# Kernel optimization log

Measured on AMD Instinct MI355X. Metric: run time of the kernel, lower is better.

Reference implementation:

```python
import jax, jax.numpy as jnp
import numpy as np

B, S, D, H = 2, 2048, 1024, 16
DK = D // H


def setup_inputs() -> dict:
    key = jax.random.key(0)
    ks = jax.random.split(key, 8)
    q = jax.random.normal(ks[0], (B, S, D), dtype=jnp.float32)
    k = jax.random.normal(ks[1], (B, S, D), dtype=jnp.float32)
    v = jax.random.normal(ks[2], (B, S, D), dtype=jnp.float32)
    mask = jax.random.randint(ks[3], (B, 1, S, S), 0, 2, dtype=jnp.int32)
    sc = 1.0 / np.sqrt(D)
    Wq = jax.random.normal(ks[4], (D, D), dtype=jnp.float32) * sc
    Wk = jax.random.normal(ks[5], (D, D), dtype=jnp.float32) * sc
    Wv = jax.random.normal(ks[6], (D, D), dtype=jnp.float32) * sc
    Wo = jax.random.normal(ks[7], (D, D), dtype=jnp.float32) * sc
    return {"q": q, "k": k, "v": v, "mask": mask, "Wq": Wq, "Wk": Wk, "Wv": Wv, "Wo": Wo}


def reference(q, k, v, mask, Wq, Wk, Wv, Wo):
    # Linear projections (torch Linear: x @ W.T; bias=False). Weights here stored
    # as [D, D] applied as x @ W (equivalent parameterization).
    query = q @ Wq  # [B,S,D]
    key = k @ Wk
    value = v @ Wv
    # split heads -> [B,H,S,DK]
    query = query.reshape(B, S, H, DK).transpose(0, 2, 1, 3)
    key = key.reshape(B, S, H, DK).transpose(0, 2, 1, 3)
    value = value.reshape(B, S, H, DK).transpose(0, 2, 1, 3)
    scores = jnp.einsum('bhqd,bhkd->bhqk', query, key) / jnp.sqrt(jnp.float32(DK))
    scores = jnp.where(mask == 0, jnp.float32(-1e9), scores)
    probs = jax.nn.softmax(scores, axis=-1)  # dropout p=0.0 -> identity
    x = jnp.einsum('bhqk,bhkd->bhqd', probs, value)
    x = x.transpose(0, 2, 1, 3).reshape(B, S, D)
    return x @ Wo
```

## Files before the change

kernel.cpp:

```cpp
#include <hip/hip_runtime.h>
#include <hip/hip_bf16.h>
#include <math.h>

#define B_ 2
#define S_ 2048
#define D_ 1024
#define H_ 16
#define DK_ 64
#define SW_ (S_ / 64)

typedef unsigned short u16;
typedef unsigned int u32;
typedef unsigned long long u64;
typedef __attribute__((ext_vector_type(8))) short short8;
typedef __attribute__((ext_vector_type(4))) float float4_;
typedef __attribute__((ext_vector_type(4))) unsigned int uint4_;

static __device__ inline u16 f_to_bf16(float f) {
    union { float f; u32 i; } x; x.f = f;
    u32 r = x.i + 0x7fff + ((x.i >> 16) & 1);
    return (u16)(r >> 16);
}

static __device__ __forceinline__ u32 pack2(float a, float b) {
    union { float f; u32 i; } xa, xb; xa.f = a; xb.f = b;
    return ((xa.i + 0x8000u) >> 16) | ((xb.i + 0x8000u) & 0xffff0000u);
}

static __device__ __forceinline__ u32 cvtpk(float a, float b) {
    u32 r;
    asm("v_cvt_pk_bf16_f32 %0, %1, %2" : "=v"(r) : "v"(a), "v"(b));
    return r;
}

static __device__ __forceinline__ float fast_exp2(float x) {
#if __has_builtin(__builtin_amdgcn_exp2f)
    return __builtin_amdgcn_exp2f(x);
#else
    return exp2f(x);
#endif
}

static __device__ inline void gl_lds16(const u16* g, u16* l) {
    __builtin_amdgcn_global_load_lds((const __attribute__((address_space(1))) void*)g,
                                     (__attribute__((address_space(3))) void*)l, 16, 0, 0);
}

__global__ __launch_bounds__(256) void prep(const float* __restrict__ q,
                                            const float* __restrict__ k,
                                            const float* __restrict__ v,
                                            const int* __restrict__ mask,
                                            const float* __restrict__ W0,
                                            const float* __restrict__ W1,
                                            const float* __restrict__ W2,
                                            const float* __restrict__ W3,
                                            u16* __restrict__ qb, u16* __restrict__ kb,
                                            u16* __restrict__ vb,
                                            u16* __restrict__ T0, u16* __restrict__ T1,
                                            u16* __restrict__ T2, u16* __restrict__ T3,
                                            u64* __restrict__ mpk) {
    __shared__ float tile[32][33];
    int gx = blockIdx.x, tid = threadIdx.x;
    if (gx < 6144) {
        int z = gx >> 11;
        int bx = gx & 2047;
        const float* s = (z == 0) ? q : ((z == 1) ? k : v);
        u16* d = (z == 0) ? qb : ((z == 1) ? kb : vb);
        int i = (bx * 256 + tid) * 8;
        #pragma unroll
        for (int j = 0; j < 8; ++j) d[i + j] = f_to_bf16(s[i + j]);
    } else if (gx < 10240) {
        int g2 = gx - 6144;
        int z = g2 >> 10;
        int rem = g2 & 1023;
        const float* W = (z == 0) ? W0 : ((z == 1) ? W1 : ((z == 2) ? W2 : W3));
        u16* Wt = (z == 0) ? T0 : ((z == 1) ? T1 : ((z == 2) ? T2 : T3));
        int k0 = (rem >> 5) * 32, n0 = (rem & 31) * 32;
        int tx = tid & 31, ty = tid >> 5;
        #pragma unroll
        for (int i2 = 0; i2 < 4; ++i2) {
            int row = ty + i2 * 8;
            tile[row][tx] = W[(size_t)(k0 + row) * D_ + n0 + tx];
        }
        __syncthreads();
        #pragma unroll
        for (int i2 = 0; i2 < 4; ++i2) {
            int row = ty + i2 * 8;
            Wt[(size_t)(n0 + row) * D_ + k0 + tx] = f_to_bf16(tile[tx][row]);
        }
    } else {
        int g3 = gx - 10240;
        int wv = (g3 * 256 + tid) >> 6;
        int lane = tid & 63;
        #pragma unroll
        for (int i2 = 0; i2 < 8; ++i2) {
            int wd = wv * 8 + i2;
            u64 bits = __ballot(mask[(size_t)wd * 64 + lane] != 0);
            if (lane == 0) mpk[wd] = bits;
        }
    }
}

static __device__ __forceinline__ void gemm128_body(u16* lds,
                                                    const u16* __restrict__ A,
                                                    const u16* __restrict__ Bt,
                                                    int K, float4_ (&acc)[4][4]) {
    u16* ldsA = lds;
    u16* ldsB = lds + 4096;
    int tm = blockIdx.x, tn = blockIdx.y;
    int t = threadIdx.x, l = t & 63;
    int w = t >> 6, wr = w >> 1, wc = w & 1;
    int colL = l & 15, grp = l >> 4;
    int sw4 = (grp ^ ((colL >> 1) & 3)) << 3;
    int f0 = t, f1 = t + 256;
    int row0 = f0 >> 2, kc0 = (((f0 & 3) ^ ((f0 >> 3) & 3)) << 3);
    int row1 = f1 >> 2, kc1 = (((f1 & 3) ^ ((f1 >> 3) & 3)) << 3);
    const u16* gA0 = A  + (size_t)(tm * 128 + row0) * K + kc0;
    const u16* gA1 = A  + (size_t)(tm * 128 + row1) * K + kc1;
    const u16* gB0 = Bt + (size_t)(tn * 128 + row0) * K + kc0;
    const u16* gB1 = Bt + (size_t)(tn * 128 + row1) * K + kc1;

    #pragma unroll
    for (int mi = 0; mi < 4; ++mi)
        #pragma unroll
        for (int ni = 0; ni < 4; ++ni)
            acc[mi][ni] = (float4_){0.f, 0.f, 0.f, 0.f};

    for (int k0 = 0; k0 < K; k0 += 32) {
        __syncthreads();
        gl_lds16(gA0 + k0, ldsA + f0 * 8);
        gl_lds16(gA1 + k0, ldsA + f1 * 8);
        gl_lds16(gB0 + k0, ldsB + f0 * 8);
        gl_lds16(gB1 + k0, ldsB + f1 * 8);
        __syncthreads();
        short8 a[4], b[4];
        #pragma unroll
        for (int mi = 0; mi < 4; ++mi)
            a[mi] = *(const short8*)&ldsA[(wr * 64 + mi * 16 + colL) * 32 + sw4];
        #pragma unroll
        for (int ni = 0; ni < 4; ++ni)
            b[ni] = *(const short8*)&ldsB[(wc * 64 + ni * 16 + colL) * 32 + sw4];
        #pragma unroll
        for (int mi = 0; mi < 4; ++mi)
            #pragma unroll
            for (int ni = 0; ni < 4; ++ni)
                acc[mi][ni] = __builtin_amdgcn_mfma_f32_16x16x32_bf16(a[mi], b[ni], acc[mi][ni], 0, 0, 0);
    }
}

__global__ __launch_bounds__(256, 3) void gemm_qkv(const u16* __restrict__ qb,
                                                   const u16* __restrict__ kb,
                                                   const u16* __restrict__ vb,
                                                   const u16* __restrict__ Wqt,
                                                   const u16* __restrict__ Wkt,
                                                   const u16* __restrict__ Wvt,
                                                   u16* __restrict__ Qp,
                                                   u16* __restrict__ Kp,
                                                   u16* __restrict__ Vt) {
    __shared__ u16 lds[8192];
    int z = blockIdx.z;
    const u16* A  = (z == 0) ? qb  : ((z == 1) ? kb  : vb);
    const u16* Bt = (z == 0) ? Wqt : ((z == 1) ? Wkt : Wvt);
    float4_ acc[4][4];
    gemm128_body(lds, A, Bt, D_, acc);

    int tm = blockIdx.x, tn = blockIdx.y;
    int t = threadIdx.x, l = t & 63;
    int w = t >> 6, wr = w >> 1, wc = w & 1;
    int colL = l & 15, grp = l >> 4;

    if (z < 2) {
        u16* Y = (z == 0) ? Qp : Kp;
        float sc = (z == 0) ? (0.125f * 1.44269504f) : 1.0f;
        #pragma unroll
        for (int mi = 0; mi < 4; ++mi)
            #pragma unroll
            for (int ni = 0; ni < 4; ++ni)
                #pragma unroll
                for (int r = 0; r < 4; ++r)
                    Y[(size_t)(tm * 128 + wr * 64 + mi * 16 + grp * 4 + r) * D_
                      + tn * 128 + wc * 64 + ni * 16 + colL] = f_to_bf16(acc[mi][ni][r] * sc);
    } else {
        int tok_base = tm * 128 + wr * 64;
        int bb = tok_base >> 11;
        int s_hi = tok_base & (S_ - 1);
        #pragma unroll
        for (int mi = 0; mi < 4; ++mi)
            #pragma unroll
            for (int ni = 0; ni < 4; ++ni) {
                int n  = tn * 128 + wc * 64 + ni * 16 + colL;
                int hh = n >> 6, dk = n & 63;
                u16* vp = Vt + ((size_t)(bb * H_ + hh) * DK_ + dk) * S_ + s_hi;
                #pragma unroll
                for (int r = 0; r < 4; ++r) {
                    int m = mi * 16 + grp * 4 + r;
                    int mp_ = ((m >> 5) & 1) * 32 + ((m >> 2) & 3) * 8 + ((m >> 4) & 1) * 4 + (m & 3);
                    vp[mp_] = f_to_bf16(acc[mi][ni][r]);
                }
            }
    }
}

__global__ __launch_bounds__(256, 3) void gemm_out(const u16* __restrict__ Xa,
                                                   const u16* __restrict__ Wot,
                                                   float* __restrict__ out) {
    __shared__ u16 lds[8192];
    float4_ acc[4][4];
    gemm128_body(lds, Xa, Wot, out ? (int)D_ : (int)D_, acc);

    int tm = blockIdx.x, tn = blockIdx.y;
    int t = threadIdx.x, l = t & 63;
    int w = t >> 6, wr = w >> 1, wc = w & 1;
    int colL = l & 15, grp = l >> 4;
    #pragma unroll
    for (int mi = 0; mi < 4; ++mi)
        #pragma unroll
        for (int ni = 0; ni < 4; ++ni)
            #pragma unroll
            for (int r = 0; r < 4; ++r)
                out[(size_t)(tm * 128 + wr * 64 + mi * 16 + grp * 4 + r) * D_
                    + tn * 128 + wc * 64 + ni * 16 + colL] = acc[mi][ni][r];
}

__global__ __launch_bounds__(256, 4) void attn128(const u16* __restrict__ Qp,
                                                  const u16* __restrict__ Kp,
                                                  const u16* __restrict__ Vt,
                                                  const u64* __restrict__ mp,
                                                  u16* __restrict__ Xa) {
    __shared__ u16 ldsK[128 * 64];
    __shared__ u16 ldsV[2 * 64 * 64];

    int bid = blockIdx.x;
    int qt = bid & 31, h = (bid >> 5) & 15, b = bid >> 9;
    int t = threadIdx.x, l = t & 63, w = t >> 6;
    int colL = l & 15, grp = l >> 4;

    const u16* qbase = Qp + (size_t)(b * S_ + qt * 64 + w * 16 + colL) * D_ + h * DK_;
    short8 qf0 = *(const short8*)(qbase + grp * 8);
    short8 qf1 = *(const short8*)(qbase + 32 + grp * 8);

    const u16* gK[4];
    const u16* gV[4];
    #pragma unroll
    for (int i = 0; i < 4; ++i) {
        int f = t + 256 * i;
        int krow = f >> 3, kch = (((f & 7) ^ (krow & 7)) << 3);
        gK[i] = Kp + (size_t)(b * S_ + krow) * D_ + h * DK_ + kch;
        int hreg = f >> 9, fp = f & 511;
        int vrow = fp >> 3, vch = (((fp & 7) ^ (vrow & 7)) << 3);
        gV[i] = Vt + ((size_t)(b * H_ + h) * DK_ + vrow) * S_ + hreg * 64 + vch;
    }

    int sw8 = (grp ^ (colL & 7)) << 3;

    short8 onesb;
    #pragma unroll
    for (int j = 0; j < 8; ++j) onesb[j] = (short)0x3F80;

    float4_ lacc = (float4_){0.f, 0.f, 0.f, 0.f};
    float4_ o[4];
    #pragma unroll
    for (int nt = 0; nt < 4; ++nt) o[nt] = (float4_){0.f, 0.f, 0.f, 0.f};

    const u64* mrow = mp + (size_t)(b * S_ + qt * 64 + w * 16 + colL) * SW_;

    for (int kt = 0; kt < S_; kt += 128) {
        u64 mw0 = mrow[(kt >> 6)];
        u64 mw1 = mrow[(kt >> 6) + 1];

        __syncthreads();
        #pragma unroll
        for (int i = 0; i < 4; ++i) {
            int f = t + 256 * i;
            gl_lds16(gK[i] + (size_t)kt * D_, ldsK + f * 8);
            gl_lds16(gV[i] + kt,              ldsV + f * 8);
        }
        __syncthreads();

        float4_ s[8];
        __builtin_amdgcn_s_setprio(1);
        #pragma unroll
        for (int nt = 0; nt < 8; ++nt) {
            int ro = (nt * 16 + colL) * 64;
            short8 kf0 = *(const short8*)&ldsK[ro + sw8];
            short8 kf1 = *(const short8*)&ldsK[ro + (sw8 ^ 32)];
            s[nt] = (float4_){0.f, 0.f, 0.f, 0.f};
            s[nt] = __builtin_amdgcn_mfma_f32_16x16x32_bf16(kf0, qf0, s[nt], 0, 0, 0);
            s[nt] = __builtin_amdgcn_mfma_f32_16x16x32_bf16(kf1, qf1, s[nt], 0, 0, 0);
        }
        __builtin_amdgcn_s_setprio(0);

        u64 msh0 = mw0 >> (grp * 4), msh1 = mw1 >> (grp * 4);
        #pragma unroll
        for (int nt = 0; nt < 8; ++nt) {
            u64 msh = (nt < 4) ? msh0 : msh1;
            #pragma unroll
            for (int r = 0; r < 4; ++r) {
                float p = fast_exp2(s[nt][r]);
                u32 keep = 0u - (u32)((msh >> ((nt & 3) * 16 + r)) & 1ull);
                union { float f; u32 i; } pu; pu.f = p;
                pu.i &= keep;
                s[nt][r] = pu.f;
            }
        }

        short8 pf[4];
        #pragma unroll
        for (int j = 0; j < 4; ++j) {
            uint4_ Ax = { cvtpk(s[2 * j][0], s[2 * j][1]), cvtpk(s[2 * j][2], s[2 * j][3]),
                          cvtpk(s[2 * j + 1][0], s[2 * j + 1][1]), cvtpk(s[2 * j + 1][2], s[2 * j + 1][3]) };
            pf[j] = __builtin_bit_cast(short8, Ax);
        }

        __builtin_amdgcn_s_setprio(1);
        #pragma unroll
        for (int nt = 0; nt < 4; ++nt) {
            int ro = (nt * 16 + colL) * 64;
            short8 vf0 = *(const short8*)&ldsV[ro + sw8];
            short8 vf1 = *(const short8*)&ldsV[ro + (sw8 ^ 32)];
            short8 vf2 = *(const short8*)&ldsV[4096 + ro + sw8];
            short8 vf3 = *(const short8*)&ldsV[4096 + ro + (sw8 ^ 32)];
            o[nt] = __builtin_amdgcn_mfma_f32_16x16x32_bf16(pf[0], vf0, o[nt], 0, 0, 0);
            o[nt] = __builtin_amdgcn_mfma_f32_16x16x32_bf16(pf[1], vf1, o[nt], 0, 0, 0);
            o[nt] = __builtin_amdgcn_mfma_f32_16x16x32_bf16(pf[2], vf2, o[nt], 0, 0, 0);
            o[nt] = __builtin_amdgcn_mfma_f32_16x16x32_bf16(pf[3], vf3, o[nt], 0, 0, 0);
        }
        lacc = __builtin_amdgcn_mfma_f32_16x16x32_bf16(pf[0], onesb, lacc, 0, 0, 0);
        lacc = __builtin_amdgcn_mfma_f32_16x16x32_bf16(pf[1], onesb, lacc, 0, 0, 0);
        lacc = __builtin_amdgcn_mfma_f32_16x16x32_bf16(pf[2], onesb, lacc, 0, 0, 0);
        lacc = __builtin_amdgcn_mfma_f32_16x16x32_bf16(pf[3], onesb, lacc, 0, 0, 0);
        __builtin_amdgcn_s_setprio(0);
    }

    float inv[4];
    #pragma unroll
    for (int r = 0; r < 4; ++r) inv[r] = 1.f / lacc[r];

    u16* xo = Xa + (size_t)(b * S_ + qt * 64 + w * 16 + grp * 4) * D_ + h * DK_;
    #pragma unroll
    for (int r = 0; r < 4; ++r)
        #pragma unroll
        for (int nt = 0; nt < 4; ++nt)
            xo[(size_t)r * D_ + nt * 16 + colL] = f_to_bf16(o[nt][r] * inv[r]);
}

extern "C" void kernel_launch(void* const* d_in, const int* in_sizes, int n_in,
                              void* d_out, int out_size, void* d_ws, size_t ws_size,
                              hipStream_t stream) {
    const float* q    = (const float*)d_in[0];
    const float* k    = (const float*)d_in[1];
    const float* v    = (const float*)d_in[2];
    const int*   mask = (const int*)d_in[3];
    const float* Wq   = (const float*)d_in[4];
    const float* Wk   = (const float*)d_in[5];
    const float* Wv   = (const float*)d_in[6];
    const float* Wo   = (const float*)d_in[7];
    float* out = (float*)d_out;

    const int NQ = B_ * S_ * D_;
    const int NW = D_ * D_;

    u16* qb  = (u16*)d_ws;
    u16* kb  = qb  + NQ;
    u16* vb  = kb  + NQ;
    u16* Wqt = vb  + NQ;
    u16* Wkt = Wqt + NW;
    u16* Wvt = Wkt + NW;
    u16* Wot = Wvt + NW;
    u16* Qp  = Wot + NW;
    u16* Kp  = Qp  + NQ;
    u16* Vt  = Kp  + NQ;
    u16* Xa  = Vt  + NQ;
    u64* mpk = (u64*)(Xa + NQ);

    dim3 cblk(256);
    prep<<<14336, cblk, 0, stream>>>(q, k, v, mask, Wq, Wk, Wv, Wo,
                                     qb, kb, vb, Wqt, Wkt, Wvt, Wot, mpk);

    const int M = B_ * S_;
    gemm_qkv<<<dim3(M / 128, D_ / 128, 3), cblk, 0, stream>>>(qb, kb, vb, Wqt, Wkt, Wvt, Qp, Kp, Vt);

    attn128<<<B_ * H_ * (S_ / 64), cblk, 0, stream>>>(Qp, Kp, Vt, mpk, Xa);

    gemm_out<<<dim3(M / 128, D_ / 128), cblk, 0, stream>>>(Xa, Wot, out);
}
```

Before: 253.7 us.

## Process 128 query rows per attention block to reuse K/V tiles

Each wave now computes two 16-row query groups against the same K and V fragments loaded from shared memory. This halves K/V global-to-LDS loads and LDS fragment reads per query row, and halves the grid size. It doubles accumulator register use, and launch bounds drop to 2 blocks per CU, which reduces occupancy and the number of blocks available to fill the GPU.

```diff
diff --git a/kernel.cpp b/kernel.cpp
--- a/kernel.cpp
+++ b/kernel.cpp
@@ -20,11 +20,6 @@
     union { float f; u32 i; } x; x.f = f;
     u32 r = x.i + 0x7fff + ((x.i >> 16) & 1);
     return (u16)(r >> 16);
-}
-
-static __device__ __forceinline__ u32 pack2(float a, float b) {
-    union { float f; u32 i; } xa, xb; xa.f = a; xb.f = b;
-    return ((xa.i + 0x8000u) >> 16) | ((xb.i + 0x8000u) & 0xffff0000u);
 }
 
 static __device__ __forceinline__ u32 cvtpk(float a, float b) {
@@ -206,7 +201,7 @@
                                                    float* __restrict__ out) {
     __shared__ u16 lds[8192];
     float4_ acc[4][4];
-    gemm128_body(lds, Xa, Wot, out ? (int)D_ : (int)D_, acc);
+    gemm128_body(lds, Xa, Wot, D_, acc);
 
     int tm = blockIdx.x, tn = blockIdx.y;
     int t = threadIdx.x, l = t & 63;
@@ -222,7 +217,7 @@
                     + tn * 128 + wc * 64 + ni * 16 + colL] = acc[mi][ni][r];
 }
 
-__global__ __launch_bounds__(256, 4) void attn128(const u16* __restrict__ Qp,
+__global__ __launch_bounds__(256, 2) void attn128(const u16* __restrict__ Qp,
                                                   const u16* __restrict__ Kp,
                                                   const u16* __restrict__ Vt,
                                                   const u64* __restrict__ mp,
@@ -231,13 +226,16 @@
     __shared__ u16 ldsV[2 * 64 * 64];
 
     int bid = blockIdx.x;
-    int qt = bid & 31, h = (bid >> 5) & 15, b = bid >> 9;
+    int qt = bid & 15, h = (bid >> 4) & 15, b = bid >> 8;
     int t = threadIdx.x, l = t & 63, w = t >> 6;
     int colL = l & 15, grp = l >> 4;
 
-    const u16* qbase = Qp + (size_t)(b * S_ + qt * 64 + w * 16 + colL) * D_ + h * DK_;
-    short8 qf0 = *(const short8*)(qbase + grp * 8);
-    short8 qf1 = *(const short8*)(qbase + 32 + grp * 8);
+    const u16* qbA = Qp + (size_t)(b * S_ + qt * 128 + w * 32 + colL) * D_ + h * DK_;
+    const u16* qbB = qbA + (size_t)16 * D_;
+    short8 qfA0 = *(const short8*)(qbA + grp * 8);
+    short8 qfA1 = *(const short8*)(qbA + 32 + grp * 8);
+    short8 qfB0 = *(const short8*)(qbB + grp * 8);
+    short8 qfB1 = *(const short8*)(qbB + 32 + grp * 8);
 
     const u16* gK[4];
     const u16* gV[4];
@@ -257,16 +255,23 @@
     #pragma unroll
     for (int j = 0; j < 8; ++j) onesb[j] = (short)0x3F80;
 
-    float4_ lacc = (float4_){0.f, 0.f, 0.f, 0.f};
-    float4_ o[4];
-    #pragma unroll
-    for (int nt = 0; nt < 4; ++nt) o[nt] = (float4_){0.f, 0.f, 0.f, 0.f};
-
-    const u64* mrow = mp + (size_t)(b * S_ + qt * 64 + w * 16 + colL) * SW_;
+    float4_ laccA = (float4_){0.f, 0.f, 0.f, 0.f};
+    float4_ laccB = (float4_){0.f, 0.f, 0.f, 0.f};
+    float4_ oA[4], oB[4];
+    #pragma unroll
+    for (int nt = 0; nt < 4; ++nt) {
+        oA[nt] = (float4_){0.f, 0.f, 0.f, 0.f};
+        oB[nt] = (float4_){0.f, 0.f, 0.f, 0.f};
+    }
+
+    const u64* mrA = mp + (size_t)(b * S_ + qt * 128 + w * 32 + colL) * SW_;
+    const u64* mrB = mrA + (size_t)16 * SW_;
 
     for (int kt = 0; kt < S_; kt += 128) {
-        u64 mw0 = mrow[(kt >> 6)];
-        u64 mw1 = mrow[(kt >> 6) + 1];
+        u64 mwA0 = mrA[(kt >> 6)];
+        u64 mwA1 = mrA[(kt >> 6) + 1];
+        u64 mwB0 = mrB[(kt >> 6)];
+        u64 mwB1 = mrB[(kt >> 6) + 1];
 
         __syncthreads();
         #pragma unroll
@@ -277,39 +282,49 @@
         }
         __syncthreads();
 
-        float4_ s[8];
+        float4_ sA[8], sB[8];
         __builtin_amdgcn_s_setprio(1);
         #pragma unroll
         for (int nt = 0; nt < 8; ++nt) {
             int ro = (nt * 16 + colL) * 64;
             short8 kf0 = *(const short8*)&ldsK[ro + sw8];
             short8 kf1 = *(const short8*)&ldsK[ro + (sw8 ^ 32)];
-            s[nt] = (float4_){0.f, 0.f, 0.f, 0.f};
-            s[nt] = __builtin_amdgcn_mfma_f32_16x16x32_bf16(kf0, qf0, s[nt], 0, 0, 0);
-            s[nt] = __builtin_amdgcn_mfma_f32_16x16x32_bf16(kf1, qf1, s[nt], 0, 0, 0);
+            sA[nt] = (float4_){0.f, 0.f, 0.f, 0.f};
+            sA[nt] = __builtin_amdgcn_mfma_f32_16x16x32_bf16(kf0, qfA0, sA[nt], 0, 0, 0);
+            sA[nt] = __builtin_amdgcn_mfma_f32_16x16x32_bf16(kf1, qfA1, sA[nt], 0, 0, 0);
+            sB[nt] = (float4_){0.f, 0.f, 0.f, 0.f};
+            sB[nt] = __builtin_amdgcn_mfma_f32_16x16x32_bf16(kf0, qfB0, sB[nt], 0, 0, 0);
+            sB[nt] = __builtin_amdgcn_mfma_f32_16x16x32_bf16(kf1, qfB1, sB[nt], 0, 0, 0);
         }
         __builtin_amdgcn_s_setprio(0);
 
-        u64 msh0 = mw0 >> (grp * 4), msh1 = mw1 >> (grp * 4);
+        u64 mshA0 = mwA0 >> (grp * 4), mshA1 = mwA1 >> (grp * 4);
+        u64 mshB0 = mwB0 >> (grp * 4), mshB1 = mwB1 >> (grp * 4);
         #pragma unroll
         for (int nt = 0; nt < 8; ++nt) {
-            u64 msh = (nt < 4) ? msh0 : msh1;
+            u32 bitsA = ((u32)((nt < 4 ? mshA0 : mshA1) >> ((nt & 3) * 16))) & 15u;
+            u32 bitsB = ((u32)((nt < 4 ? mshB0 : mshB1) >> ((nt & 3) * 16))) & 15u;
             #pragma unroll
             for (int r = 0; r < 4; ++r) {
-                float p = fast_exp2(s[nt][r]);
-                u32 keep = 0u - (u32)((msh >> ((nt & 3) * 16 + r)) & 1ull);
-                union { float f; u32 i; } pu; pu.f = p;
-                pu.i &= keep;
-                s[nt][r] = pu.f;
+                float pA = fast_exp2(sA[nt][r]);
+                float pB = fast_exp2(sB[nt][r]);
+                u32 keepA = 0u - ((bitsA >> r) & 1u);
+                u32 keepB = 0u - ((bitsB >> r) & 1u);
+                union { float f; u32 i; } ua, ub;
+                ua.f = pA; ua.i &= keepA; sA[nt][r] = ua.f;
+                ub.f = pB; ub.i &= keepB; sB[nt][r] = ub.f;
             }
         }
 
-        short8 pf[4];
+        short8 pfA[4], pfB[4];
         #pragma unroll
         for (int j = 0; j < 4; ++j) {
-            uint4_ Ax = { cvtpk(s[2 * j][0], s[2 * j][1]), cvtpk(s[2 * j][2], s[2 * j][3]),
-                          cvtpk(s[2 * j + 1][0], s[2 * j + 1][1]), cvtpk(s[2 * j + 1][2], s[2 * j + 1][3]) };
-            pf[j] = __builtin_bit_cast(short8, Ax);
+            uint4_ Ax = { cvtpk(sA[2 * j][0], sA[2 * j][1]), cvtpk(sA[2 * j][2], sA[2 * j][3]),
+                          cvtpk(sA[2 * j + 1][0], sA[2 * j + 1][1]), cvtpk(sA[2 * j + 1][2], sA[2 * j + 1][3]) };
+            pfA[j] = __builtin_bit_cast(short8, Ax);
+            uint4_ Bx = { cvtpk(sB[2 * j][0], sB[2 * j][1]), cvtpk(sB[2 * j][2], sB[2 * j][3]),
+                          cvtpk(sB[2 * j + 1][0], sB[2 * j + 1][1]), cvtpk(sB[2 * j + 1][2], sB[2 * j + 1][3]) };
+            pfB[j] = __builtin_bit_cast(short8, Bx);
         }
 
         __builtin_amdgcn_s_setprio(1);
@@ -320,28 +335,42 @@
             short8 vf1 = *(const short8*)&ldsV[ro + (sw8 ^ 32)];
             short8 vf2 = *(const short8*)&ldsV[4096 + ro + sw8];
             short8 vf3 = *(const short8*)&ldsV[4096 + ro + (sw8 ^ 32)];
-            o[nt] = __builtin_amdgcn_mfma_f32_16x16x32_bf16(pf[0], vf0, o[nt], 0, 0, 0);
-            o[nt] = __builtin_amdgcn_mfma_f32_16x16x32_bf16(pf[1], vf1, o[nt], 0, 0, 0);
-            o[nt] = __builtin_amdgcn_mfma_f32_16x16x32_bf16(pf[2], vf2, o[nt], 0, 0, 0);
-            o[nt] = __builtin_amdgcn_mfma_f32_16x16x32_bf16(pf[3], vf3, o[nt], 0, 0, 0);
-        }
-        lacc = __builtin_amdgcn_mfma_f32_16x16x32_bf16(pf[0], onesb, lacc, 0, 0, 0);
-        lacc = __builtin_amdgcn_mfma_f32_16x16x32_bf16(pf[1], onesb, lacc, 0, 0, 0);
-        lacc = __builtin_amdgcn_mfma_f32_16x16x32_bf16(pf[2], onesb, lacc, 0, 0, 0);
-        lacc = __builtin_amdgcn_mfma_f32_16x16x32_bf16(pf[3], onesb, lacc, 0, 0, 0);
+            oA[nt] = __builtin_amdgcn_mfma_f32_16x16x32_bf16(pfA[0], vf0, oA[nt], 0, 0, 0);
+            oA[nt] = __builtin_amdgcn_mfma_f32_16x16x32_bf16(pfA[1], vf1, oA[nt], 0, 0, 0);
+            oA[nt] = __builtin_amdgcn_mfma_f32_16x16x32_bf16(pfA[2], vf2, oA[nt], 0, 0, 0);
+            oA[nt] = __builtin_amdgcn_mfma_f32_16x16x32_bf16(pfA[3], vf3, oA[nt], 0, 0, 0);
+            oB[nt] = __builtin_amdgcn_mfma_f32_16x16x32_bf16(pfB[0], vf0, oB[nt], 0, 0, 0);
+            oB[nt] = __builtin_amdgcn_mfma_f32_16x16x32_bf16(pfB[1], vf1, oB[nt], 0, 0, 0);
+            oB[nt] = __builtin_amdgcn_mfma_f32_16x16x32_bf16(pfB[2], vf2, oB[nt], 0, 0, 0);
+            oB[nt] = __builtin_amdgcn_mfma_f32_16x16x32_bf16(pfB[3], vf3, oB[nt], 0, 0, 0);
+        }
+        laccA = __builtin_amdgcn_mfma_f32_16x16x32_bf16(pfA[0], onesb, laccA, 0, 0, 0);
+        laccA = __builtin_amdgcn_mfma_f32_16x16x32_bf16(pfA[1], onesb, laccA, 0, 0, 0);
+        laccA = __builtin_amdgcn_mfma_f32_16x16x32_bf16(pfA[2], onesb, laccA, 0, 0, 0);
+        laccA = __builtin_amdgcn_mfma_f32_16x16x32_bf16(pfA[3], onesb, laccA, 0, 0, 0);
+        laccB = __builtin_amdgcn_mfma_f32_16x16x32_bf16(pfB[0], onesb, laccB, 0, 0, 0);
+        laccB = __builtin_amdgcn_mfma_f32_16x16x32_bf16(pfB[1], onesb, laccB, 0, 0, 0);
+        laccB = __builtin_amdgcn_mfma_f32_16x16x32_bf16(pfB[2], onesb, laccB, 0, 0, 0);
+        laccB = __builtin_amdgcn_mfma_f32_16x16x32_bf16(pfB[3], onesb, laccB, 0, 0, 0);
         __builtin_amdgcn_s_setprio(0);
     }
 
-    float inv[4];
-    #pragma unroll
-    for (int r = 0; r < 4; ++r) inv[r] = 1.f / lacc[r];
-
-    u16* xo = Xa + (size_t)(b * S_ + qt * 64 + w * 16 + grp * 4) * D_ + h * DK_;
+    float invA[4], invB[4];
+    #pragma unroll
+    for (int r = 0; r < 4; ++r) {
+        invA[r] = 1.f / laccA[r];
+        invB[r] = 1.f / laccB[r];
+    }
+
+    u16* xoA = Xa + (size_t)(b * S_ + qt * 128 + w * 32 + grp * 4) * D_ + h * DK_;
+    u16* xoB = xoA + (size_t)16 * D_;
     #pragma unroll
     for (int r = 0; r < 4; ++r)
         #pragma unroll
-        for (int nt = 0; nt < 4; ++nt)
-            xo[(size_t)r * D_ + nt * 16 + colL] = f_to_bf16(o[nt][r] * inv[r]);
+        for (int nt = 0; nt < 4; ++nt) {
+            xoA[(size_t)r * D_ + nt * 16 + colL] = f_to_bf16(oA[nt][r] * invA[r]);
+            xoB[(size_t)r * D_ + nt * 16 + colL] = f_to_bf16(oB[nt][r] * invB[r]);
+        }
 }
 
 extern "C" void kernel_launch(void* const* d_in, const int* in_sizes, int n_in,
@@ -380,7 +409,7 @@
     const int M = B_ * S_;
     gemm_qkv<<<dim3(M / 128, D_ / 128, 3), cblk, 0, stream>>>(qb, kb, vb, Wqt, Wkt, Wvt, Qp, Kp, Vt);
 
-    attn128<<<B_ * H_ * (S_ / 64), cblk, 0, stream>>>(Qp, Kp, Vt, mpk, Xa);
+    attn128<<<B_ * H_ * (S_ / 128), cblk, 0, stream>>>(Qp, Kp, Vt, mpk, Xa);
 
     gemm_out<<<dim3(M / 128, D_ / 128), cblk, 0, stream>>>(Xa, Wot, out);
 }
```

New measurement: 242.4 us. -4.5%, faster.
